# Optimization experiments

Hardware: AMD Instinct MI355X
Metric: run time of the kernel (lower is better)

Reference implementation:

```python
import jax, jax.numpy as jnp
import numpy as np

IMG_H, IMG_W = 180, 320
SIGMA = 30.0
COEFF = 0.8
MAXPOINTS = 5
KSIZE = int(4 * SIGMA + 1)
if KSIZE % 2 == 0:
    KSIZE += 1  # 121
PAD = KSIZE // 2  # 60
B, T = 16, 64


def _make_kernel_1d():
    x = jnp.arange(KSIZE, dtype=jnp.float32) - (KSIZE // 2)
    k = jnp.exp(-x ** 2 / (2.0 * SIGMA ** 2))
    return k / k.sum()


def setup_inputs() -> dict:
    key = jax.random.key(0)
    gaze_coords = jax.random.uniform(key, (B, T, MAXPOINTS * 2), dtype=jnp.float32)
    kernel_1d = _make_kernel_1d()
    return {"gaze_coords": gaze_coords, "kernel_1d": kernel_1d}


def _conv(x, k, pad):
    # x: [N,1,H,W], k: [1,1,kh,kw], pad: ((ph,ph),(pw,pw))
    return jax.lax.conv_general_dilated(
        x, k, window_strides=(1, 1), padding=pad,
        dimension_numbers=("NCHW", "OIHW", "NCHW"))


def reference(gaze_coords, kernel_1d):
    Bv, Tv, _ = gaze_coords.shape
    coords = gaze_coords.reshape(Bv, Tv, MAXPOINTS, 2)  # b t p 2
    H, W = IMG_H, IMG_W

    valid = (coords[..., 0] >= 0) & (coords[..., 1] >= 0)  # [b,t,p]
    x_idx = (jnp.clip(coords[..., 0], 0.0, 1.0) * (W - 1)).astype(jnp.int32)
    x_idx = jnp.clip(x_idx, 0, W - 1)
    y_idx = (jnp.clip(coords[..., 1], 0.0, 1.0) * (H - 1)).astype(jnp.int32)
    y_idx = jnp.clip(y_idx, 0, H - 1)

    rank = jnp.cumsum(valid.astype(jnp.int32), axis=2) - 1
    rank = jnp.clip(rank, 0).astype(jnp.float32)
    weights = jnp.power(jnp.float32(COEFF), rank) * valid.astype(jnp.float32)

    N = Bv * Tv
    lin_idx = (y_idx * W + x_idx).reshape(N, MAXPOINTS)
    w_flat = weights.reshape(N, MAXPOINTS)
    delta = jnp.zeros((N, H * W), dtype=jnp.float32)
    delta = delta.at[jnp.arange(N)[:, None], lin_idx].add(w_flat)
    delta = delta.reshape(N, 1, H, W)

    # Faithful to original: vertical (Lx1) kernel with horizontal padding,
    # then horizontal (1xL) kernel with vertical padding.
    k_v = kernel_1d.reshape(1, 1, KSIZE, 1)
    k_h = kernel_1d.reshape(1, 1, 1, KSIZE)
    blurred = _conv(delta, k_v, ((0, 0), (PAD, PAD)))     # [N,1,H-K+1,W+2P]
    blurred = _conv(blurred, k_h, ((PAD, PAD), (0, 0)))   # [N,1,H,W]

    max_vals = jnp.max(blurred, axis=(2, 3), keepdims=True)
    normalized = blurred / (max_vals + 1e-8)
    return normalized.reshape(Bv, Tv, 1, H, W)
```

## Files before the change

kernel.cpp:

```cpp
#include <hip/hip_runtime.h>


namespace {
constexpr int IMG_H   = 180;
constexpr int IMG_W   = 320;
constexpr int KSIZE   = 121;
constexpr int PAD     = 60;
constexpr int MAXP    = 5;
constexpr int MID0    = 60;
constexpr int MIDR    = 60;
constexpr int W4      = IMG_W / 4;
constexpr int FRAMEQ  = IMG_H * W4;
constexpr int BLOCK   = 320;
constexpr int NW      = BLOCK / 64;
constexpr int GROUPS  = 4;
constexpr int ROWS_PT = MIDR / GROUPS;
}

typedef float vfloat4 __attribute__((ext_vector_type(4)));

__global__ __launch_bounds__(BLOCK) void gaze_kernel(
    const float* __restrict__ coords,
    const float* __restrict__ k1d,
    float* __restrict__ out,
    int nframes)
{
    const int bid = blockIdx.x;
    const int tid = threadIdx.x;

    if (bid >= nframes) {
        const int f = bid - nframes;
        vfloat4* o = (vfloat4*)out + (size_t)f * FRAMEQ;
        const vfloat4 z = (vfloat4)(0.0f);
        #pragma unroll
        for (int i = 0; i < 15; ++i) {
            o[tid + i * BLOCK] = z;
            o[9600 + tid + i * BLOCK] = z;
        }
        return;
    }

    __shared__ float sK[KSIZE];
    __shared__ float sC[MAXP * 2];
    __shared__ float sColW[MAXP][IMG_W];
    __shared__ float sRowK[MAXP][MIDR];
    __shared__ float sWaveMax[NW];

    const int f   = bid;
    const int wq  = tid % W4;
    const int grp = tid / W4;

    if (tid < KSIZE) sK[tid] = k1d[tid];
    if (tid >= KSIZE && tid < KSIZE + MAXP * 2)
        sC[tid - KSIZE] = coords[(long)f * (MAXP * 2) + (tid - KSIZE)];
    __syncthreads();

    int xi[MAXP], yi[MAXP];
    float wt[MAXP];
    {
        int cum = 0;
        #pragma unroll
        for (int p = 0; p < MAXP; ++p) {
            float x = sC[2 * p], y = sC[2 * p + 1];
            bool valid = (x >= 0.0f) && (y >= 0.0f);
            float xf = fminf(fmaxf(x, 0.0f), 1.0f) * (float)(IMG_W - 1);
            float yf = fminf(fmaxf(y, 0.0f), 1.0f) * (float)(IMG_H - 1);
            int xq = (int)xf; xq = xq < 0 ? 0 : (xq > IMG_W - 1 ? IMG_W - 1 : xq);
            int yq = (int)yf; yq = yq < 0 ? 0 : (yq > IMG_H - 1 ? IMG_H - 1 : yq);
            cum += valid ? 1 : 0;
            int rk = cum - 1; if (rk < 0) rk = 0;
            float w = 1.0f;
            for (int r = 0; r < rk; ++r) w *= 0.8f;
            xi[p] = xq; yi[p] = yq; wt[p] = valid ? w : 0.0f;
        }
    }
    #pragma unroll
    for (int p = 0; p < MAXP; ++p) {
        int idx = xi[p] - tid + PAD;
        sColW[p][tid] = (idx >= 0 && idx < KSIZE) ? sK[idx] * wt[p] : 0.0f;
    }
    if (tid < MAXP * MIDR) {
        int p = tid / MIDR, g = tid - p * MIDR;
        int idx = yi[p] - g;
        sRowK[p][g] = (idx >= 0 && idx < KSIZE) ? sK[idx] : 0.0f;
    }
    __syncthreads();

    vfloat4 cv0 = ((const vfloat4*)sColW[0])[wq];
    vfloat4 cv1 = ((const vfloat4*)sColW[1])[wq];
    vfloat4 cv2 = ((const vfloat4*)sColW[2])[wq];
    vfloat4 cv3 = ((const vfloat4*)sColW[3])[wq];
    vfloat4 cv4 = ((const vfloat4*)sColW[4])[wq];
    vfloat4 vals[ROWS_PT];
    float lmax = 0.0f;
    #pragma unroll
    for (int i = 0; i < ROWS_PT; ++i) {
        int g = i * 4 + grp;
        vfloat4 a;
        a  = sRowK[0][g] * cv0;
        a += sRowK[1][g] * cv1;
        a += sRowK[2][g] * cv2;
        a += sRowK[3][g] * cv3;
        a += sRowK[4][g] * cv4;
        vals[i] = a;
        lmax = fmaxf(lmax, fmaxf(fmaxf(a.x, a.y), fmaxf(a.z, a.w)));
    }

    #pragma unroll
    for (int off = 32; off >= 1; off >>= 1)
        lmax = fmaxf(lmax, __shfl_xor(lmax, off, 64));
    if ((tid & 63) == 0) sWaveMax[tid >> 6] = lmax;
    __syncthreads();
    float m = sWaveMax[0];
    #pragma unroll
    for (int wv = 1; wv < NW; ++wv) m = fmaxf(m, sWaveMax[wv]);
    const float inv = 1.0f / (m + 1e-8f);

    vfloat4* out4 = (vfloat4*)out + (size_t)f * FRAMEQ;
    #pragma unroll
    for (int i = 0; i < ROWS_PT; ++i) {
        vfloat4 v = vals[i] * inv;
        out4[(MID0 + i * 4 + grp) * W4 + wq] = v;
    }
}

extern "C" void kernel_launch(void* const* d_in, const int* in_sizes, int n_in,
                              void* d_out, int out_size, void* d_ws, size_t ws_size,
                              hipStream_t stream) {
    const float* coords = (const float*)d_in[0];
    const float* k1d    = (const float*)d_in[1];
    float* out          = (float*)d_out;
    const int N = in_sizes[0] / (MAXP * 2);
    gaze_kernel<<<2 * N, BLOCK, 0, stream>>>(coords, k1d, out, N);
}
```

Measured before the change: 40.63 us.

## Split zero-fill across blocks and overlap stores with setup; recompute outputs

Compute blocks now write the top 60 zero rows of their own frame at the start, before the shared-memory setup, and the extra blocks only zero the bottom 60 rows. This overlaps global stores with the coefficient loads and makes the block types carry similar amounts of work. __syncthreads is replaced by a raw s_barrier that waits only on LDS counters, so pending global stores do not hold up the barrier. Outputs are recomputed after the max reduction instead of being kept in 60 registers, which lowers register pressure at the cost of extra LDS reads and FMAs.

```diff
diff --git a/kernel.cpp b/kernel.cpp
--- a/kernel.cpp
+++ b/kernel.cpp
@@ -13,11 +13,16 @@
 constexpr int FRAMEQ  = IMG_H * W4;
 constexpr int BLOCK   = 320;
 constexpr int NW      = BLOCK / 64;
-constexpr int GROUPS  = 4;
-constexpr int ROWS_PT = MIDR / GROUPS;
+constexpr int ROWS_PT = 15;
 }
 
 typedef float vfloat4 __attribute__((ext_vector_type(4)));
+
+__device__ __forceinline__ void raw_barrier_lgkm() {
+    asm volatile("s_waitcnt lgkmcnt(0)" ::: "memory");
+    __builtin_amdgcn_s_barrier();
+    __builtin_amdgcn_sched_barrier(0);
+}
 
 __global__ __launch_bounds__(BLOCK) void gaze_kernel(
     const float* __restrict__ coords,
@@ -29,14 +34,11 @@
     const int tid = threadIdx.x;
 
     if (bid >= nframes) {
-        const int f = bid - nframes;
-        vfloat4* o = (vfloat4*)out + (size_t)f * FRAMEQ;
+        vfloat4* o = (vfloat4*)out + (size_t)(bid - nframes) * FRAMEQ + 9600;
         const vfloat4 z = (vfloat4)(0.0f);
         #pragma unroll
-        for (int i = 0; i < 15; ++i) {
+        for (int i = 0; i < ROWS_PT; ++i)
             o[tid + i * BLOCK] = z;
-            o[9600 + tid + i * BLOCK] = z;
-        }
         return;
     }
 
@@ -50,10 +52,21 @@
     const int wq  = tid % W4;
     const int grp = tid / W4;
 
-    if (tid < KSIZE) sK[tid] = k1d[tid];
-    if (tid >= KSIZE && tid < KSIZE + MAXP * 2)
-        sC[tid - KSIZE] = coords[(long)f * (MAXP * 2) + (tid - KSIZE)];
-    __syncthreads();
+    float kreg = 0.0f, creg = 0.0f;
+    if (tid < KSIZE) kreg = k1d[tid];
+    if (tid >= 128 && tid < 128 + MAXP * 2)
+        creg = coords[(long)f * (MAXP * 2) + (tid - 128)];
+
+    vfloat4* out4 = (vfloat4*)out + (size_t)f * FRAMEQ;
+    const vfloat4 z = (vfloat4)(0.0f);
+    #pragma unroll
+    for (int i = 0; i < ROWS_PT; ++i)
+        out4[(i * 4 + grp) * W4 + wq] = z;
+    __builtin_amdgcn_sched_barrier(0);
+
+    if (tid < KSIZE) sK[tid] = kreg;
+    if (tid >= 128 && tid < 128 + MAXP * 2) sC[tid - 128] = creg;
+    raw_barrier_lgkm();
 
     int xi[MAXP], yi[MAXP];
     float wt[MAXP];
@@ -84,14 +97,13 @@
         int idx = yi[p] - g;
         sRowK[p][g] = (idx >= 0 && idx < KSIZE) ? sK[idx] : 0.0f;
     }
-    __syncthreads();
+    raw_barrier_lgkm();
 
     vfloat4 cv0 = ((const vfloat4*)sColW[0])[wq];
     vfloat4 cv1 = ((const vfloat4*)sColW[1])[wq];
     vfloat4 cv2 = ((const vfloat4*)sColW[2])[wq];
     vfloat4 cv3 = ((const vfloat4*)sColW[3])[wq];
     vfloat4 cv4 = ((const vfloat4*)sColW[4])[wq];
-    vfloat4 vals[ROWS_PT];
     float lmax = 0.0f;
     #pragma unroll
     for (int i = 0; i < ROWS_PT; ++i) {
@@ -102,25 +114,28 @@
         a += sRowK[2][g] * cv2;
         a += sRowK[3][g] * cv3;
         a += sRowK[4][g] * cv4;
-        vals[i] = a;
         lmax = fmaxf(lmax, fmaxf(fmaxf(a.x, a.y), fmaxf(a.z, a.w)));
     }
-
     #pragma unroll
     for (int off = 32; off >= 1; off >>= 1)
         lmax = fmaxf(lmax, __shfl_xor(lmax, off, 64));
     if ((tid & 63) == 0) sWaveMax[tid >> 6] = lmax;
-    __syncthreads();
+    raw_barrier_lgkm();
     float m = sWaveMax[0];
     #pragma unroll
     for (int wv = 1; wv < NW; ++wv) m = fmaxf(m, sWaveMax[wv]);
     const float inv = 1.0f / (m + 1e-8f);
 
-    vfloat4* out4 = (vfloat4*)out + (size_t)f * FRAMEQ;
     #pragma unroll
     for (int i = 0; i < ROWS_PT; ++i) {
-        vfloat4 v = vals[i] * inv;
-        out4[(MID0 + i * 4 + grp) * W4 + wq] = v;
+        int g = i * 4 + grp;
+        vfloat4 a;
+        a  = sRowK[0][g] * cv0;
+        a += sRowK[1][g] * cv1;
+        a += sRowK[2][g] * cv2;
+        a += sRowK[3][g] * cv3;
+        a += sRowK[4][g] * cv4;
+        out4[(MID0 + g) * W4 + wq] = a * inv;
     }
 }
 
```

Result: faster. 35.49 us (-12.7%).
